# Kernel tuning notes

Hardware: AMD Instinct MI355X
Metric: run time of the kernel (lower is better)

Reference implementation:

```python
import jax, jax.numpy as jnp
import numpy as np

EMBED_DIM = 1024
NUM_HEADS = 16


def setup_inputs() -> dict:
    key = jax.random.key(0)
    kx, kq, kk, kv, ko = jax.random.split(key, 5)
    B, S, D = 2, 2048, EMBED_DIM
    s = 1.0 / np.sqrt(D)
    return {
        "x": jax.random.normal(kx, (B, S, D), dtype=jnp.float32),
        "Wq": jax.random.normal(kq, (D, D), dtype=jnp.float32) * s,
        "Wk": jax.random.normal(kk, (D, D), dtype=jnp.float32) * s,
        "Wv": jax.random.normal(kv, (D, D), dtype=jnp.float32) * s,
        "Wo": jax.random.normal(ko, (D, D), dtype=jnp.float32) * s,
    }


def reference(x, Wq, Wk, Wv, Wo):
    B, S, D = x.shape
    H = NUM_HEADS
    d_k = D // H
    # QKV projections (nn.Linear applies x @ W.T)
    q = (x @ Wq.T).reshape(B, S, H, d_k).transpose(0, 2, 1, 3)  # [B,H,S,d_k]
    k = (x @ Wk.T).reshape(B, S, H, d_k).transpose(0, 2, 1, 3)
    v = (x @ Wv.T).reshape(B, S, H, d_k).transpose(0, 2, 1, 3)
    scores = jnp.einsum("bhqd,bhkd->bhqk", q, k) / jnp.sqrt(jnp.float32(d_k))
    probs = jax.nn.softmax(scores, axis=-1)  # dropout is identity in eval
    attn = jnp.einsum("bhqk,bhkd->bhqd", probs, v)  # [B,H,S,d_k]
    attn = attn.transpose(0, 2, 1, 3).reshape(B, S, D)
    return attn @ Wo.T
```

## Files before the change

### kernel.cpp

```cpp
#include <hip/hip_runtime.h>
#include <stdint.h>

typedef __attribute__((ext_vector_type(4))) float    f32x4;
typedef __attribute__((ext_vector_type(8))) _Float16 half8;
typedef __attribute__((ext_vector_type(4))) _Float16 half4;
typedef unsigned long long u64;

#define MFMA16(a, b, c)    __builtin_amdgcn_mfma_f32_16x16x32_f16(a, b, c, 0, 0, 0)
#define MFMA16K16(a, b, c) __builtin_amdgcn_mfma_f32_16x16x16f16(a, b, c, 0, 0, 0)

#if __has_builtin(__builtin_amdgcn_exp2f)
#define EXP2F(x) __builtin_amdgcn_exp2f(x)
#else
#define EXP2F(x) exp2f(x)
#endif

#define CEXP 0.18033688f

__device__ inline void gl_lds16(const void* g, void* l) {
    __builtin_amdgcn_global_load_lds(
        (const __attribute__((address_space(1))) unsigned int*)g,
        (__attribute__((address_space(3))) unsigned int*)l, 16, 0, 0);
}

__global__ __launch_bounds__(256) void cast_all(
    const float* __restrict__ x,  const float* __restrict__ wq,
    const float* __restrict__ wk, const float* __restrict__ wv,
    const float* __restrict__ wo,
    _Float16* __restrict__ xh,  _Float16* __restrict__ wqh,
    _Float16* __restrict__ wkh, _Float16* __restrict__ wvh,
    _Float16* __restrict__ woh) {
    const int NX = 4194304, NW = 1048576;
    int i = (blockIdx.x * 256 + threadIdx.x) * 4;
    const float* src; _Float16* dst; int off;
    if (i < NX) { src = x; dst = xh; off = i; }
    else {
        int j = i - NX; int w = j >> 20; off = j & (NW - 1);
        src = (w == 0) ? wq : (w == 1) ? wk : (w == 2) ? wv : wo;
        dst = (w == 0) ? wqh : (w == 1) ? wkh : (w == 2) ? wvh : woh;
    }
    f32x4 v = *(const f32x4*)(src + off);
    half4 o;
    o.x = (_Float16)v.x; o.y = (_Float16)v.y; o.z = (_Float16)v.z; o.w = (_Float16)v.w;
    *(half4*)(dst + off) = o;
}

#define BN 128
#define BK 64

template <int MODE>
__global__ __launch_bounds__(256) void gemm_bt(const _Float16* __restrict__ A,
                                               const _Float16* __restrict__ B,
                                               void* __restrict__ C0,
                                               void* __restrict__ C1,
                                               void* __restrict__ C2,
                                               int M, int N, int K) {
    constexpr int BM  = (MODE == 3) ? 128 : 64;
    constexpr int MT  = BM / 32;
    constexpr int AIT = BM / 32;

    __shared__ __attribute__((aligned(16))) _Float16 smem[(BM + BN) * BK];
    _Float16* As = smem;
    _Float16* Bs = smem + BM * BK;

    const int tid  = threadIdx.x;
    const int wave = tid >> 6;
    const int lane = tid & 63;
    const int l16  = lane & 15;
    const int quad = lane >> 4;
    const int m0 = blockIdx.y * BM;
    const int n0 = blockIdx.x * BN;
    const int wm = (wave >> 1) * (BM / 2);
    const int wn = (wave & 1) * 64;

    const int srow = tid >> 3;
    const int scc  = (tid & 7) ^ ((tid >> 3) & 7);

    f32x4 acc[MT][4];
#pragma unroll
    for (int i = 0; i < MT; i++)
#pragma unroll
        for (int j = 0; j < 4; j++) acc[i][j] = (f32x4){0.f, 0.f, 0.f, 0.f};

    for (int k0 = 0; k0 < K; k0 += BK) {
        __syncthreads();
#pragma unroll
        for (int i = 0; i < AIT; i++)
            gl_lds16(A + (size_t)(m0 + i * 32 + srow) * K + k0 + scc * 8,
                     (char*)As + i * 4096 + wave * 1024);
#pragma unroll
        for (int i = 0; i < 4; i++)
            gl_lds16(B + (size_t)(n0 + i * 32 + srow) * K + k0 + scc * 8,
                     (char*)Bs + i * 4096 + wave * 1024);
        __syncthreads();

#pragma unroll
        for (int kk = 0; kk < 2; kk++) {
            half8 af[MT], bf[4];
#pragma unroll
            for (int mt = 0; mt < MT; mt++) {
                int row = wm + mt * 16 + l16;
                af[mt] = *(const half8*)(As + row * 64 + ((quad + 4 * kk) ^ (row & 7)) * 8);
            }
#pragma unroll
            for (int nt = 0; nt < 4; nt++) {
                int row = wn + nt * 16 + l16;
                bf[nt] = *(const half8*)(Bs + row * 64 + ((quad + 4 * kk) ^ (row & 7)) * 8);
            }
#pragma unroll
            for (int mt = 0; mt < MT; mt++)
#pragma unroll
                for (int nt = 0; nt < 4; nt++)
                    acc[mt][nt] = MFMA16(af[mt], bf[nt], acc[mt][nt]);
        }
    }

    if (MODE == 0) {
        float* C = (float*)C0;
#pragma unroll
        for (int mt = 0; mt < MT; mt++)
#pragma unroll
            for (int r = 0; r < 4; r++) {
                int row = m0 + wm + mt * 16 + quad * 4 + r;
                float* Crow = C + (size_t)row * N + n0 + wn + l16;
#pragma unroll
                for (int nt = 0; nt < 4; nt++) Crow[nt * 16] = acc[mt][nt][r];
            }
    } else {
        const int region = n0 >> 10;
        const int nb = (n0 & 1023) + wn;
        if (region < 2) {
            _Float16* C = (region == 0) ? (_Float16*)C0 : (_Float16*)C1;
            const float scale = (region == 0) ? CEXP : 1.f;
#pragma unroll
            for (int mt = 0; mt < MT; mt++)
#pragma unroll
                for (int r = 0; r < 4; r++) {
                    int mg = m0 + wm + mt * 16 + quad * 4 + r;
                    int b = mg >> 11, s = mg & 2047;
#pragma unroll
                    for (int nt = 0; nt < 4; nt++) {
                        int nw = nb + nt * 16 + l16;
                        int h = nw >> 6, d = nw & 63;
                        C[(((size_t)b * 16 + h) * 2048 + s) * 64 + d] =
                            (_Float16)(acc[mt][nt][r] * scale);
                    }
                }
        } else {
            __syncthreads();
            _Float16* ep = smem + wave * 4096;
#pragma unroll
            for (int mt = 0; mt < MT; mt++)
#pragma unroll
                for (int nt = 0; nt < 4; nt++) {
                    int dn = nt * 16 + l16;
                    int slot = (mt * 2 + (quad >> 1)) ^ (dn & 7);
                    union { half4 h; u64 q; } o;
#pragma unroll
                    for (int r = 0; r < 4; r++) o.h[r] = (_Float16)acc[mt][nt][r];
                    *(u64*)(ep + dn * 64 + slot * 8 + (quad & 1) * 4) = o.q;
                }
            __syncthreads();
            int mgb = m0 + wm;
            int b = mgb >> 11, sbase = mgb & 2047;
            int h = nb >> 6;
            _Float16* C = (_Float16*)C2 + ((size_t)b * 16 + h) * 64 * 2048;
#pragma unroll
            for (int j = 0; j < 8; j++) {
                int dn = j * 8 + (lane >> 3);
                int slot = (lane & 7) ^ (dn & 7);
                half8 val = *(const half8*)(ep + dn * 64 + slot * 8);
                *(half8*)(C + (size_t)dn * 2048 + sbase + (lane & 7) * 8) = val;
            }
        }
    }
}

__global__ __launch_bounds__(256) void attn_kernel(const _Float16* __restrict__ Q,
                                                   const _Float16* __restrict__ Kg,
                                                   const _Float16* __restrict__ Vt,
                                                   _Float16* __restrict__ Oa) {
    __shared__ __attribute__((aligned(16))) _Float16 Ks[64 * 64];
    __shared__ __attribute__((aligned(16))) _Float16 Vs[64 * 68];

    const int tid  = threadIdx.x;
    const int wave = tid >> 6;
    const int lane = tid & 63;
    const int l16  = lane & 15;
    const int quad = lane >> 4;
    const int bh = blockIdx.y;
    const int q0 = blockIdx.x * 128 + wave * 32;

    half8 qf[2][2];
#pragma unroll
    for (int qt = 0; qt < 2; qt++)
#pragma unroll
        for (int kk = 0; kk < 2; kk++)
            qf[qt][kk] = *(const half8*)(Q + ((size_t)bh * 2048 + q0 + qt * 16 + l16) * 64 +
                                         (quad + 4 * kk) * 8);

    const int srow = tid >> 3;
    const int sc8  = tid & 7;
    const int kslot = sc8 ^ (srow & 7);

    const _Float16* kp = Kg + (size_t)bh * 2048 * 64 + (size_t)srow * 64 + sc8 * 8;
    const _Float16* vp = Vt + (size_t)bh * 64 * 2048 + (size_t)srow * 2048 + sc8 * 8;

    f32x4 lsum4[2];
    f32x4 oacc[2][4];
#pragma unroll
    for (int qt = 0; qt < 2; qt++) {
        lsum4[qt] = (f32x4){0.f, 0.f, 0.f, 0.f};
#pragma unroll
        for (int dt = 0; dt < 4; dt++) oacc[qt][dt] = (f32x4){0.f, 0.f, 0.f, 0.f};
    }

    half8 kr0 = *(const half8*)(kp);
    half8 kr1 = *(const half8*)(kp + 32 * 64);
    half8 vr0 = *(const half8*)(vp);
    half8 vr1 = *(const half8*)(vp + 32 * 2048);

    for (int kt = 0; kt < 2048; kt += 64) {
        __syncthreads();
        *(half8*)(Ks + srow * 64 + kslot * 8) = kr0;
        *(half8*)(Ks + (srow + 32) * 64 + kslot * 8) = kr1;
        {
            union { half8 h; u64 q[2]; } u0, u1;
            u0.h = vr0; u1.h = vr1;
            _Float16* vd0 = Vs + srow * 68 + sc8 * 8;
            _Float16* vd1 = Vs + (srow + 32) * 68 + sc8 * 8;
            *(u64*)(vd0) = u0.q[0]; *(u64*)(vd0 + 4) = u0.q[1];
            *(u64*)(vd1) = u1.q[0]; *(u64*)(vd1 + 4) = u1.q[1];
        }
        __syncthreads();

        {
            int kt2 = (kt + 64) & 2047;
            kr0 = *(const half8*)(kp + (size_t)kt2 * 64);
            kr1 = *(const half8*)(kp + (size_t)(kt2 + 32) * 64);
            vr0 = *(const half8*)(vp + kt2);
            vr1 = *(const half8*)(vp + 32 * 2048 + kt2);
        }

        f32x4 sc4[2][4];
#pragma unroll
        for (int nt = 0; nt < 4; nt++) {
            int row = nt * 16 + l16;
            half8 kf0 = *(const half8*)(Ks + row * 64 + (quad ^ (row & 7)) * 8);
            half8 kf1 = *(const half8*)(Ks + row * 64 + ((quad + 4) ^ (row & 7)) * 8);
#pragma unroll
            for (int qt = 0; qt < 2; qt++) {
                f32x4 s = (f32x4){0.f, 0.f, 0.f, 0.f};
                s = MFMA16(kf0, qf[qt][0], s);
                s = MFMA16(kf1, qf[qt][1], s);
                sc4[qt][nt] = s;
            }
        }

        half4 ph[2][4];
#pragma unroll
        for (int qt = 0; qt < 2; qt++)
#pragma unroll
            for (int nt = 0; nt < 4; nt++) {
                half4 p;
#pragma unroll
                for (int r = 0; r < 4; r++) {
                    float pe = EXP2F(sc4[qt][nt][r]);
                    lsum4[qt][r] += pe;
                    p[r] = (_Float16)pe;
                }
                ph[qt][nt] = p;
            }

#pragma unroll
        for (int nt = 0; nt < 4; nt++) {
#pragma unroll
            for (int dt = 0; dt < 4; dt++) {
                int row = dt * 16 + l16;
                half4 vf = *(const half4*)(Vs + row * 68 + nt * 16 + quad * 4);
#pragma unroll
                for (int qt = 0; qt < 2; qt++)
                    oacc[qt][dt] = MFMA16K16(vf, ph[qt][nt], oacc[qt][dt]);
            }
        }
    }

    const int b = bh >> 4, h = bh & 15;
#pragma unroll
    for (int qt = 0; qt < 2; qt++) {
        float ls = (lsum4[qt][0] + lsum4[qt][1]) + (lsum4[qt][2] + lsum4[qt][3]);
        ls += __shfl_xor(ls, 16);
        ls += __shfl_xor(ls, 32);
        float inv = 1.f / ls;
        int q = q0 + qt * 16 + l16;
        _Float16* orow = Oa + ((size_t)b * 2048 + q) * 1024 + h * 64;
#pragma unroll
        for (int dt = 0; dt < 4; dt++) {
            half4 o;
#pragma unroll
            for (int r = 0; r < 4; r++) o[r] = (_Float16)(oacc[qt][dt][r] * inv);
            *(half4*)(orow + dt * 16 + quad * 4) = o;
        }
    }
}

extern "C" void kernel_launch(void* const* d_in, const int* in_sizes, int n_in,
                              void* d_out, int out_size, void* d_ws, size_t ws_size,
                              hipStream_t stream) {
    const float* x  = (const float*)d_in[0];
    const float* Wq = (const float*)d_in[1];
    const float* Wk = (const float*)d_in[2];
    const float* Wv = (const float*)d_in[3];
    const float* Wo = (const float*)d_in[4];
    float* out = (float*)d_out;

    const int NX = 2 * 2048 * 1024;
    const int NW = 1024 * 1024;

    _Float16* ws  = (_Float16*)d_ws;
    _Float16* xh  = ws;
    _Float16* wqh = xh + NX;
    _Float16* wkh = wqh + NW;
    _Float16* wvh = wkh + NW;
    _Float16* woh = wvh + NW;
    _Float16* Qb  = woh + NW;
    _Float16* Kb  = Qb + NX;
    _Float16* Vtb = Kb + NX;
    _Float16* Ab  = Vtb + NX;

    cast_all<<<8192, 256, 0, stream>>>(x, Wq, Wk, Wv, Wo, xh, wqh, wkh, wvh, woh);

    gemm_bt<3><<<dim3(3072 / 128, 4096 / 128), 256, 0, stream>>>(
        xh, wqh, Qb, Kb, Vtb, 4096, 3072, 1024);

    attn_kernel<<<dim3(16, 32), 256, 0, stream>>>(Qb, Kb, Vtb, Ab);

    gemm_bt<0><<<dim3(1024 / 128, 4096 / 64), 256, 0, stream>>>(
        Ab, woh, out, nullptr, nullptr, 4096, 1024, 1024);
}
```

Measured before the change: 191.8 us.

## Replace LDS staging with register prefetch in GEMM and direct loads in attention

The GEMM drops the global_load_lds async copies in favour of register-prefetched global loads that are stored into swizzled LDS, with the next tile loaded while the current one computes. The Q/K projection epilogue now stages through padded LDS so the head-major output is written with coalesced 16-byte stores instead of scattered 2-byte stores. The attention kernel removes shared memory and barriers entirely, loading K and V fragments straight from global memory into registers, and swaps the grid so blocks of the same batch-head launch adjacently for cache locality. This trades LDS reuse for more global/L2 traffic and higher register pressure in attention.

Result: slower. 313.8 us (+63.6%).

```diff
diff --git a/kernel.cpp b/kernel.cpp
--- a/kernel.cpp
+++ b/kernel.cpp
@@ -4,6 +4,7 @@
 typedef __attribute__((ext_vector_type(4))) float    f32x4;
 typedef __attribute__((ext_vector_type(8))) _Float16 half8;
 typedef __attribute__((ext_vector_type(4))) _Float16 half4;
+typedef uint32_t __attribute__((may_alias)) u32a;
 typedef unsigned long long u64;
 
 #define MFMA16(a, b, c)    __builtin_amdgcn_mfma_f32_16x16x32_f16(a, b, c, 0, 0, 0)
@@ -17,10 +18,11 @@
 
 #define CEXP 0.18033688f
 
-__device__ inline void gl_lds16(const void* g, void* l) {
-    __builtin_amdgcn_global_load_lds(
-        (const __attribute__((address_space(1))) unsigned int*)g,
-        (__attribute__((address_space(3))) unsigned int*)l, 16, 0, 0);
+__device__ inline half8 lds_read8_a4(const _Float16* p) {
+    union { u32a u[4]; half8 h; } v;
+    const u32a* q = (const u32a*)p;
+    v.u[0] = q[0]; v.u[1] = q[1]; v.u[2] = q[2]; v.u[3] = q[3];
+    return v.h;
 }
 
 __global__ __launch_bounds__(256) void cast_all(
@@ -58,8 +60,9 @@
     constexpr int BM  = (MODE == 3) ? 128 : 64;
     constexpr int MT  = BM / 32;
     constexpr int AIT = BM / 32;
-
-    __shared__ __attribute__((aligned(16))) _Float16 smem[(BM + BN) * BK];
+    constexpr int SMEMN = (MODE == 3) ? 16896 : (BM + BN) * BK;
+
+    __shared__ __attribute__((aligned(16))) _Float16 smem[SMEMN];
     _Float16* As = smem;
     _Float16* Bs = smem + BM * BK;
 
@@ -74,25 +77,39 @@
     const int wn = (wave & 1) * 64;
 
     const int srow = tid >> 3;
-    const int scc  = (tid & 7) ^ ((tid >> 3) & 7);
+    const int g8   = tid & 7;
+    const int slot = g8 ^ (srow & 7);
+
+    const _Float16* Ap = A + (size_t)(m0 + srow) * K + g8 * 8;
+    const _Float16* Bp = B + (size_t)(n0 + srow) * K + g8 * 8;
 
     f32x4 acc[MT][4];
 #pragma unroll
     for (int i = 0; i < MT; i++)
 #pragma unroll
         for (int j = 0; j < 4; j++) acc[i][j] = (f32x4){0.f, 0.f, 0.f, 0.f};
+
+    half8 ar[AIT], br[4];
+#pragma unroll
+    for (int i = 0; i < AIT; i++) ar[i] = *(const half8*)(Ap + (size_t)i * 32 * K);
+#pragma unroll
+    for (int i = 0; i < 4; i++)  br[i] = *(const half8*)(Bp + (size_t)i * 32 * K);
 
     for (int k0 = 0; k0 < K; k0 += BK) {
         __syncthreads();
 #pragma unroll
         for (int i = 0; i < AIT; i++)
-            gl_lds16(A + (size_t)(m0 + i * 32 + srow) * K + k0 + scc * 8,
-                     (char*)As + i * 4096 + wave * 1024);
+            *(half8*)(As + (i * 32 + srow) * 64 + slot * 8) = ar[i];
 #pragma unroll
         for (int i = 0; i < 4; i++)
-            gl_lds16(B + (size_t)(n0 + i * 32 + srow) * K + k0 + scc * 8,
-                     (char*)Bs + i * 4096 + wave * 1024);
+            *(half8*)(Bs + (i * 32 + srow) * 64 + slot * 8) = br[i];
         __syncthreads();
+
+        int k2 = k0 + BK; if (k2 == K) k2 = 0;
+#pragma unroll
+        for (int i = 0; i < AIT; i++) ar[i] = *(const half8*)(Ap + (size_t)i * 32 * K + k2);
+#pragma unroll
+        for (int i = 0; i < 4; i++)  br[i] = *(const half8*)(Bp + (size_t)i * 32 * K + k2);
 
 #pragma unroll
         for (int kk = 0; kk < 2; kk++) {
@@ -132,20 +149,27 @@
         if (region < 2) {
             _Float16* C = (region == 0) ? (_Float16*)C0 : (_Float16*)C1;
             const float scale = (region == 0) ? CEXP : 1.f;
+            __syncthreads();
+            _Float16* ep = smem + wave * 4224;
 #pragma unroll
             for (int mt = 0; mt < MT; mt++)
 #pragma unroll
                 for (int r = 0; r < 4; r++) {
-                    int mg = m0 + wm + mt * 16 + quad * 4 + r;
-                    int b = mg >> 11, s = mg & 2047;
-#pragma unroll
-                    for (int nt = 0; nt < 4; nt++) {
-                        int nw = nb + nt * 16 + l16;
-                        int h = nw >> 6, d = nw & 63;
-                        C[(((size_t)b * 16 + h) * 2048 + s) * 64 + d] =
-                            (_Float16)(acc[mt][nt][r] * scale);
-                    }
+                    int sr = mt * 16 + quad * 4 + r;
+#pragma unroll
+                    for (int nt = 0; nt < 4; nt++)
+                        ep[sr * 66 + nt * 16 + l16] = (_Float16)(acc[mt][nt][r] * scale);
                 }
+            int mgb = m0 + wm;
+            int b = mgb >> 11, sbase = mgb & 2047;
+            int h = nb >> 6;
+            _Float16* Cc = C + ((size_t)b * 16 + h) * 2048 * 64;
+#pragma unroll
+            for (int j = 0; j < 8; j++) {
+                int sr = j * 8 + (lane >> 3);
+                half8 v = lds_read8_a4(ep + sr * 66 + (lane & 7) * 8);
+                *(half8*)(Cc + (size_t)(sbase + sr) * 64 + (lane & 7) * 8) = v;
+            }
         } else {
             __syncthreads();
             _Float16* ep = smem + wave * 4096;
@@ -154,11 +178,11 @@
 #pragma unroll
                 for (int nt = 0; nt < 4; nt++) {
                     int dn = nt * 16 + l16;
-                    int slot = (mt * 2 + (quad >> 1)) ^ (dn & 7);
+                    int sl = (mt * 2 + (quad >> 1)) ^ (dn & 7);
                     union { half4 h; u64 q; } o;
 #pragma unroll
                     for (int r = 0; r < 4; r++) o.h[r] = (_Float16)acc[mt][nt][r];
-                    *(u64*)(ep + dn * 64 + slot * 8 + (quad & 1) * 4) = o.q;
+                    *(u64*)(ep + dn * 64 + sl * 8 + (quad & 1) * 4) = o.q;
                 }
             __syncthreads();
             int mgb = m0 + wm;
@@ -168,8 +192,8 @@
 #pragma unroll
             for (int j = 0; j < 8; j++) {
                 int dn = j * 8 + (lane >> 3);
-                int slot = (lane & 7) ^ (dn & 7);
-                half8 val = *(const half8*)(ep + dn * 64 + slot * 8);
+                int sl = (lane & 7) ^ (dn & 7);
+                half8 val = *(const half8*)(ep + dn * 64 + sl * 8);
                 *(half8*)(C + (size_t)dn * 2048 + sbase + (lane & 7) * 8) = val;
             }
         }
@@ -180,16 +204,13 @@
                                                    const _Float16* __restrict__ Kg,
                                                    const _Float16* __restrict__ Vt,
                                                    _Float16* __restrict__ Oa) {
-    __shared__ __attribute__((aligned(16))) _Float16 Ks[64 * 64];
-    __shared__ __attribute__((aligned(16))) _Float16 Vs[64 * 68];
-
     const int tid  = threadIdx.x;
     const int wave = tid >> 6;
     const int lane = tid & 63;
     const int l16  = lane & 15;
     const int quad = lane >> 4;
-    const int bh = blockIdx.y;
-    const int q0 = blockIdx.x * 128 + wave * 32;
+    const int bh = blockIdx.x;
+    const int q0 = blockIdx.y * 128 + wave * 32;
 
     half8 qf[2][2];
 #pragma unroll
@@ -199,12 +220,8 @@
             qf[qt][kk] = *(const half8*)(Q + ((size_t)bh * 2048 + q0 + qt * 16 + l16) * 64 +
                                          (quad + 4 * kk) * 8);
 
-    const int srow = tid >> 3;
-    const int sc8  = tid & 7;
-    const int kslot = sc8 ^ (srow & 7);
-
-    const _Float16* kp = Kg + (size_t)bh * 2048 * 64 + (size_t)srow * 64 + sc8 * 8;
-    const _Float16* vp = Vt + (size_t)bh * 64 * 2048 + (size_t)srow * 2048 + sc8 * 8;
+    const _Float16* Kb = Kg + (size_t)bh * 2048 * 64 + (size_t)l16 * 64 + quad * 8;
+    const _Float16* Vb = Vt + (size_t)bh * 64 * 2048 + (size_t)l16 * 2048 + quad * 4;
 
     f32x4 lsum4[2];
     f32x4 oacc[2][4];
@@ -215,74 +232,54 @@
         for (int dt = 0; dt < 4; dt++) oacc[qt][dt] = (f32x4){0.f, 0.f, 0.f, 0.f};
     }
 
-    half8 kr0 = *(const half8*)(kp);
-    half8 kr1 = *(const half8*)(kp + 32 * 64);
-    half8 vr0 = *(const half8*)(vp);
-    half8 vr1 = *(const half8*)(vp + 32 * 2048);
-
     for (int kt = 0; kt < 2048; kt += 64) {
-        __syncthreads();
-        *(half8*)(Ks + srow * 64 + kslot * 8) = kr0;
-        *(half8*)(Ks + (srow + 32) * 64 + kslot * 8) = kr1;
-        {
-            union { half8 h; u64 q[2]; } u0, u1;
-            u0.h = vr0; u1.h = vr1;
-            _Float16* vd0 = Vs + srow * 68 + sc8 * 8;
-            _Float16* vd1 = Vs + (srow + 32) * 68 + sc8 * 8;
-            *(u64*)(vd0) = u0.q[0]; *(u64*)(vd0 + 4) = u0.q[1];
-            *(u64*)(vd1) = u1.q[0]; *(u64*)(vd1 + 4) = u1.q[1];
+        half8 kf[4][2];
+#pragma unroll
+        for (int nt = 0; nt < 4; nt++) {
+            const _Float16* kr = Kb + (size_t)(kt + nt * 16) * 64;
+            kf[nt][0] = *(const half8*)(kr);
+            kf[nt][1] = *(const half8*)(kr + 32);
         }
-        __syncthreads();
-
-        {
-            int kt2 = (kt + 64) & 2047;
-            kr0 = *(const half8*)(kp + (size_t)kt2 * 64);
-            kr1 = *(const half8*)(kp + (size_t)(kt2 + 32) * 64);
-            vr0 = *(const half8*)(vp + kt2);
-            vr1 = *(const half8*)(vp + 32 * 2048 + kt2);
-        }
+        half4 vf[4][4];
+#pragma unroll
+        for (int dt = 0; dt < 4; dt++)
+#pragma unroll
+            for (int nt = 0; nt < 4; nt++)
+                vf[dt][nt] = *(const half4*)(Vb + (size_t)dt * 16 * 2048 + kt + nt * 16);
 
         f32x4 sc4[2][4];
 #pragma unroll
-        for (int nt = 0; nt < 4; nt++) {
-            int row = nt * 16 + l16;
-            half8 kf0 = *(const half8*)(Ks + row * 64 + (quad ^ (row & 7)) * 8);
-            half8 kf1 = *(const half8*)(Ks + row * 64 + ((quad + 4) ^ (row & 7)) * 8);
+        for (int nt = 0; nt < 4; nt++)
 #pragma unroll
             for (int qt = 0; qt < 2; qt++) {
                 f32x4 s = (f32x4){0.f, 0.f, 0.f, 0.f};
-                s = MFMA16(kf0, qf[qt][0], s);
-                s = MFMA16(kf1, qf[qt][1], s);
+                s = MFMA16(kf[nt][0], qf[qt][0], s);
+                s = MFMA16(kf[nt][1], qf[qt][1], s);
                 sc4[qt][nt] = s;
             }
-        }
 
         half4 ph[2][4];
 #pragma unroll
         for (int qt = 0; qt < 2; qt++)
 #pragma unroll
             for (int nt = 0; nt < 4; nt++) {
-                half4 p;
+                half4 pk;
 #pragma unroll
                 for (int r = 0; r < 4; r++) {
                     float pe = EXP2F(sc4[qt][nt][r]);
                     lsum4[qt][r] += pe;
-                    p[r] = (_Float16)pe;
+                    pk[r] = (_Float16)pe;
                 }
-                ph[qt][nt] = p;
-            }
-
-#pragma unroll
-        for (int nt = 0; nt < 4; nt++) {
-#pragma unroll
-            for (int dt = 0; dt < 4; dt++) {
-                int row = dt * 16 + l16;
-                half4 vf = *(const half4*)(Vs + row * 68 + nt * 16 + quad * 4);
+                ph[qt][nt] = pk;
+            }
+
+#pragma unroll
+        for (int nt = 0; nt < 4; nt++)
+#pragma unroll
+            for (int dt = 0; dt < 4; dt++)
 #pragma unroll
                 for (int qt = 0; qt < 2; qt++)
-                    oacc[qt][dt] = MFMA16K16(vf, ph[qt][nt], oacc[qt][dt]);
-            }
-        }
+                    oacc[qt][dt] = MFMA16K16(vf[dt][nt], ph[qt][nt], oacc[qt][dt]);
     }
 
     const int b = bh >> 4, h = bh & 15;
@@ -333,7 +330,7 @@
     gemm_bt<3><<<dim3(3072 / 128, 4096 / 128), 256, 0, stream>>>(
         xh, wqh, Qb, Kb, Vtb, 4096, 3072, 1024);
 
-    attn_kernel<<<dim3(16, 32), 256, 0, stream>>>(Qb, Kb, Vtb, Ab);
+    attn_kernel<<<dim3(32, 16), 256, 0, stream>>>(Qb, Kb, Vtb, Ab);
 
     gemm_bt<0><<<dim3(1024 / 128, 4096 / 64), 256, 0, stream>>>(
         Ab, woh, out, nullptr, nullptr, 4096, 1024, 1024);
```
